# Optimization experiments

Measured on AMD Instinct MI355X. Metric: run time of the kernel, lower is better.

Reference implementation:

```python
import jax, jax.numpy as jnp
import numpy as np


def pairwise_euclidean_distance(x, y):
    # x: [N, D], y: [K, D] -> [N, K] squared Euclidean distances
    cross = -2.0 * (x @ y.T)
    x_term = jnp.sum(x * x, axis=1, keepdims=True)      # [N, 1]
    y_term = jnp.sum(y * y, axis=1, keepdims=True).T    # [1, K]
    return cross + x_term + y_term


def quantize(z, centroids):
    # z: [B, T, D], centroids: [K, D]
    B, T, D = z.shape
    flat = z.reshape(-1, D)                              # [N, D]
    distances = pairwise_euclidean_distance(flat, centroids)
    alignment = jnp.argmin(distances, axis=1)            # [N]
    q = centroids[alignment]                             # gather [N, D]
    # straight-through estimator: grad flows to z, not centroids
    q = flat + jax.lax.stop_gradient(q - flat)
    return q.reshape(B, T, D)


def setup_inputs() -> dict:
    key = jax.random.key(0)
    ks = jax.random.split(key, 5)
    B, T, F, D, K = 16, 2048, 80, 512, 2048
    return {
        "x": jax.random.normal(ks[0], (B, T, F), dtype=jnp.float32),
        "W_enc": jax.random.normal(ks[1], (F, D), dtype=jnp.float32) * (1.0 / np.sqrt(F)),
        "b_enc": jnp.zeros((D,), dtype=jnp.float32),
        "centroids": jax.random.normal(ks[2], (K, D), dtype=jnp.float32),
        "W_dec": jax.random.normal(ks[3], (D, F), dtype=jnp.float32) * (1.0 / np.sqrt(D)),
        "b_dec": jnp.zeros((F,), dtype=jnp.float32),
    }


def reference(x, W_enc, b_enc, centroids, W_dec, b_dec):
    z = x @ W_enc + b_enc            # encoder: [B, T, D]
    zq = quantize(z, centroids)      # VQ: distance + argmin + gather
    out = zq @ W_dec + b_dec         # decoder: [B, T, F]
    return out
```

## Files before the change

### kernel.cpp

```cpp
#include <hip/hip_runtime.h>
#include <hip/hip_bf16.h>

#define N_TOK  32768
#define F_IN   80
#define D_DIM  512
#define K_CENT 2048
#define F_OUT  80
#define TM     16
#define KP     96
#define M2     0.5f
#define QSLOTS 12
#define QREC   104
#define TREC   416

typedef __attribute__((ext_vector_type(8)))  short bf16x8;
typedef __attribute__((ext_vector_type(4)))  float fx4;
typedef __attribute__((ext_vector_type(16))) float fx16;

#define AS3 __attribute__((address_space(3)))
#define AS1 __attribute__((address_space(1)))

__device__ inline unsigned short f2bf(float f) {
    unsigned u = __float_as_uint(f);
    return (unsigned short)((u + 0x7FFFu + ((u >> 16) & 1u)) >> 16);
}
__device__ inline float bf2f(unsigned short h) {
    return __uint_as_float((unsigned)h << 16);
}

__device__ inline void gll16(const unsigned short* g, unsigned short* l) {
    __builtin_amdgcn_global_load_lds((const AS1 unsigned*)g, (AS3 unsigned*)l, 16, 0, 0);
}

__device__ inline unsigned fkey(float f) {
    unsigned b = __float_as_uint(f);
    return b ^ ((b >> 31) ? 0xFFFFFFFFu : 0x80000000u);
}
__device__ inline float keyf(unsigned k) {
    unsigned b = k ^ ((k & 0x80000000u) ? 0x80000000u : 0xFFFFFFFFu);
    return __uint_as_float(b);
}

__device__ inline size_t frag_addr(int row, int k) {
    int stripe = row >> 4;
    int L = ((k >> 3) << 4) + (row & 15);
    return (size_t)stripe * 512 + L * 8 + (k & 7);
}

__device__ inline size_t frag32_addr(int row, int k) {
    int sub = (row >> 5) * 2 + ((k >> 4) & 1);
    int L = (row & 31) + ((k >> 3) & 1) * 32;
    return (size_t)sub * 512 + L * 8 + (k & 7);
}

__global__ void k_prep_all(const float* __restrict__ x, const float* __restrict__ Wenc,
                           const float* __restrict__ cent,
                           unsigned short* __restrict__ cbt, unsigned short* __restrict__ wbt,
                           unsigned short* __restrict__ xbt) {
    const int bid = blockIdx.x, tid = threadIdx.x;
    if (bid < 512) {
        int o = bid * 256 + tid;
        int n = o >> 6, ko = (o & 63) * 8;
        const float* src = cent + (size_t)n * D_DIM + ko;
        float4 v0 = *(const float4*)src;
        float4 v1 = *(const float4*)(src + 4);
        size_t tile = (size_t)((n >> 7) * 16 + (ko >> 5));
        uint4 p;
        p.x = (unsigned)f2bf(v0.x) | ((unsigned)f2bf(v0.y) << 16);
        p.y = (unsigned)f2bf(v0.z) | ((unsigned)f2bf(v0.w) << 16);
        p.z = (unsigned)f2bf(v1.x) | ((unsigned)f2bf(v1.y) << 16);
        p.w = (unsigned)f2bf(v1.z) | ((unsigned)f2bf(v1.w) << 16);
        *(uint4*)&cbt[tile * 4096 + frag_addr(n & 127, ko & 31)] = p;
    } else if (bid < 528) {
        int kt = bid - 512;
        int a0 = tid * 16;
        int s = a0 >> 9;
        int L0 = (tid * 2) & 63;
        int row0 = s * 16 + (L0 & 15);
        int kg = kt * 32 + (L0 >> 4) * 8;
        unsigned short u[16];
#pragma unroll
        for (int rr = 0; rr < 2; ++rr) {
            int row = row0 + rr;
            if (row < F_IN) {
                const float* src = Wenc + (size_t)row * D_DIM + kg;
                float4 v0 = *(const float4*)src;
                float4 v1 = *(const float4*)(src + 4);
                u[rr*8+0]=f2bf(v0.x); u[rr*8+1]=f2bf(v0.y); u[rr*8+2]=f2bf(v0.z); u[rr*8+3]=f2bf(v0.w);
                u[rr*8+4]=f2bf(v1.x); u[rr*8+5]=f2bf(v1.y); u[rr*8+6]=f2bf(v1.z); u[rr*8+7]=f2bf(v1.w);
            } else {
#pragma unroll
                for (int j = 0; j < 8; ++j) u[rr*8+j] = 0;
            }
        }
        unsigned short* dst = wbt + (size_t)kt * 4096 + a0;
#pragma unroll
        for (int j = 0; j < 16; ++j) dst[j] = u[j];
    } else {
        int o = (bid - 528) * 256 + tid;
        int m = o / 12;
        int ko = (o - m * 12) * 8;
        unsigned short u[8];
        if (ko < F_IN) {
            const float* src = x + (size_t)m * F_IN + ko;
            float4 v0 = *(const float4*)src;
            float4 v1 = *(const float4*)(src + 4);
            u[0]=f2bf(v0.x); u[1]=f2bf(v0.y); u[2]=f2bf(v0.z); u[3]=f2bf(v0.w);
            u[4]=f2bf(v1.x); u[5]=f2bf(v1.y); u[6]=f2bf(v1.z); u[7]=f2bf(v1.w);
        } else if (ko == 80) {
            u[0] = 0x3F80; u[1] = 0x3F80;
#pragma unroll
            for (int j = 2; j < 8; ++j) u[j] = 0;
        } else {
#pragma unroll
            for (int j = 0; j < 8; ++j) u[j] = 0;
        }
        int mt = m >> 7, kt = ko >> 5, row = m & 127, kl = ko & 31;
        uint4 p;
        p.x = (unsigned)u[0] | ((unsigned)u[1] << 16);
        p.y = (unsigned)u[2] | ((unsigned)u[3] << 16);
        p.z = (unsigned)u[4] | ((unsigned)u[5] << 16);
        p.w = (unsigned)u[6] | ((unsigned)u[7] << 16);
        *(uint4*)&xbt[(size_t)(mt * 3 + kt) * 4096 + frag32_addr(row, kl)] = p;
    }
}

__global__ __launch_bounds__(512) void k_gemm_g(
    const unsigned short* __restrict__ wbt, const unsigned short* __restrict__ cbt,
    unsigned short* __restrict__ Gbt) {
    __shared__ unsigned short lds[2][2][4096];
    const int tid = threadIdx.x;
    const int nt = blockIdx.x;
    const int lane = tid & 63;
    const int wave = tid >> 6;
    const int wm = wave >> 2, wn = wave & 3;

    const unsigned short* Bbase = cbt + (size_t)nt * 16 * 4096;
    const int woff = (tid & ~63) * 8;

    fx4 acc[4][2] = {};
    gll16(wbt + tid * 8, &lds[0][0][0] + woff);
    gll16(Bbase + tid * 8, &lds[0][1][0] + woff);

    int cur = 0;
    for (int kk = 0; kk < 16; ++kk) {
        __syncthreads();
        if (kk + 1 < 16) {
            gll16(wbt + (kk + 1) * 4096 + tid * 8, &lds[cur ^ 1][0][0] + woff);
            gll16(Bbase + (kk + 1) * 4096 + tid * 8, &lds[cur ^ 1][1][0] + woff);
        }
        const unsigned short* A = &lds[cur][0][0];
        const unsigned short* B = &lds[cur][1][0];
        bf16x8 a[4], b[2];
#pragma unroll
        for (int i = 0; i < 4; ++i) a[i] = *(const bf16x8*)&A[(wm * 4 + i) * 512 + lane * 8];
#pragma unroll
        for (int j = 0; j < 2; ++j) b[j] = *(const bf16x8*)&B[(wn * 2 + j) * 512 + lane * 8];
#pragma unroll
        for (int i = 0; i < 4; ++i)
#pragma unroll
            for (int j = 0; j < 2; ++j)
                acc[i][j] = __builtin_amdgcn_mfma_f32_16x16x32_bf16(a[i], b[j], acc[i][j], 0, 0, 0);
        cur ^= 1;
    }
    const int g = lane >> 4, cl = lane & 15;
#pragma unroll
    for (int j = 0; j < 2; ++j) {
        int colLoc = wn * 32 + j * 16 + cl;
#pragma unroll
        for (int i = 0; i < 4; ++i)
#pragma unroll
            for (int r = 0; r < 4; ++r) {
                int f = wm * 64 + i * 16 + g * 4 + r;
                if (f < KP) {
                    unsigned short v = (f < F_IN) ? f2bf(acc[i][j][r]) : (unsigned short)0;
                    Gbt[(size_t)(nt * 3 + (f >> 5)) * 4096 + frag32_addr(colLoc, f & 31)] = v;
                }
            }
    }
}

__global__ void k_cadjf(const float* __restrict__ cent, const float* __restrict__ benc,
                        float* __restrict__ cnorm, unsigned short* __restrict__ Gbt) {
    int wave = threadIdx.x >> 6, lane = threadIdx.x & 63;
    int k = blockIdx.x * 4 + wave;
    const float* row = cent + (size_t)k * D_DIM;
    float s = 0.f, t = 0.f;
#pragma unroll
    for (int j = 0; j < 8; ++j) {
        float c = row[lane + 64 * j];
        float b = benc[lane + 64 * j];
        s += c * c; t += b * c;
    }
#pragma unroll
    for (int off = 32; off; off >>= 1) { s += __shfl_down(s, off); t += __shfl_down(t, off); }
    if (lane == 0) {
        cnorm[k] = s;
        float v = -0.5f * (s - 2.0f * t);
        unsigned short h = f2bf(v);
        unsigned short l = f2bf(v - bf2f(h));
        int nt = k >> 7, cl = k & 127;
        size_t tb = (size_t)(nt * 3 + 2) * 4096;
        Gbt[tb + frag32_addr(cl, 16)] = h;
        Gbt[tb + frag32_addr(cl, 17)] = l;
    }
}

__global__ __launch_bounds__(256) void k_dec3(
    const float* __restrict__ cent, const float* __restrict__ Wdec,
    const float* __restrict__ bdec, float* __restrict__ dec) {
    __shared__ float cs[4][D_DIM];
    const int tid = threadIdx.x;
    const int k0 = blockIdx.x * 4;
#pragma unroll
    for (int q = 0; q < 2; ++q)
        ((float4*)cs)[q * 256 + tid] = ((const float4*)(cent + (size_t)k0 * D_DIM))[q * 256 + tid];
    __syncthreads();
    const int f = tid & 127, cg = tid >> 7;
    if (f < F_OUT) {
        const int c0 = cg * 2, c1 = cg * 2 + 1;
        float a0 = 0.f, b0 = 0.f, a1 = 0.f, b1 = 0.f;
        const float* wp = Wdec + f;
#pragma unroll 4
        for (int d = 0; d < D_DIM; d += 2) {
            float w0 = wp[(size_t)d * F_OUT];
            float w1 = wp[(size_t)(d + 1) * F_OUT];
            a0 += cs[c0][d] * w0;  b0 += cs[c0][d + 1] * w1;
            a1 += cs[c1][d] * w0;  b1 += cs[c1][d + 1] * w1;
        }
        float bd = bdec[f];
        dec[(size_t)(k0 + c0) * F_OUT + f] = a0 + b0 + bd;
        dec[(size_t)(k0 + c1) * F_OUT + f] = a1 + b1 + bd;
    }
}

__global__ __launch_bounds__(512) void k_dist3(
    const unsigned short* __restrict__ xbt, const unsigned short* __restrict__ Gbt,
    char* __restrict__ lists) {
    __shared__ unsigned short Bs[2][12288];
    __shared__ int cnt[128];
    __shared__ unsigned mxk[128];

    const int tid = threadIdx.x;
    const int bid = blockIdx.x;
    const int mt = bid >> 2, nq = bid & 3;
    const int lane = tid & 63;
    const int wave = tid >> 6;
    const int tg = wave >> 1;
    const int ch = wave & 1;
    const int col = lane & 31;
    const int hi = lane >> 5;

    if (tid < 128) { cnt[tid] = 0; mxk[tid] = 0u; }

    bf16x8 bfr[6];
    const unsigned short* Ab = xbt + (size_t)mt * 12288;
#pragma unroll
    for (int kc = 0; kc < 6; ++kc)
        bfr[kc] = *(const bf16x8*)&Ab[(kc >> 1) * 4096 + (tg * 2 + (kc & 1)) * 512 + lane * 8];

    const int woff = (tid & ~63) * 8;
    const unsigned short* Gq = Gbt + (size_t)nq * 4 * 12288;
#pragma unroll
    for (int q = 0; q < 3; ++q)
        gll16(Gq + q * 4096 + tid * 8, &Bs[0][0] + q * 4096 + woff);

    float rmax = -3.4e38f;
    int cur = 0;
    for (int t4 = 0; t4 < 4; ++t4) {
        __syncthreads();
        if (t4 + 1 < 4) {
#pragma unroll
            for (int q = 0; q < 3; ++q)
                gll16(Gq + (size_t)(t4 + 1) * 12288 + q * 4096 + tid * 8,
                      &Bs[cur ^ 1][0] + q * 4096 + woff);
        }
        const unsigned short* B = &Bs[cur][0];
        fx16 acc[2];
#pragma unroll
        for (int u = 0; u < 2; ++u)
#pragma unroll
            for (int r = 0; r < 16; ++r) acc[u][r] = 0.f;
#pragma unroll
        for (int kc = 0; kc < 6; ++kc) {
#pragma unroll
            for (int u = 0; u < 2; ++u) {
                bf16x8 a = *(const bf16x8*)&B[(kc >> 1) * 4096
                             + ((ch * 2 + u) * 2 + (kc & 1)) * 512 + lane * 8];
                acc[u] = __builtin_amdgcn_mfma_f32_32x32x16_bf16(a, bfr[kc], acc[u], 0, 0, 0);
            }
        }
        float m = acc[0][0];
#pragma unroll
        for (int r = 1; r < 16; ++r) m = fmaxf(m, acc[0][r]);
#pragma unroll
        for (int r = 0; r < 16; ++r) m = fmaxf(m, acc[1][r]);
        m = fmaxf(m, __shfl_xor(m, 32));
        rmax = fmaxf(rmax, m);
        const float th = rmax - M2;
        const int tk = tg * 32 + col;
        char* qrec = lists + (size_t)(mt * 128 + tk) * TREC + nq * QREC;
#pragma unroll
        for (int u = 0; u < 2; ++u)
#pragma unroll
            for (int r = 0; r < 16; ++r) {
                float v = acc[u][r];
                if (v >= th) {
                    int slot = atomicAdd(&cnt[tk], 1);
                    if (slot < QSLOTS) {
                        uint2 e;
                        e.x = __float_as_uint(v);
                        e.y = (unsigned)((nq * 4 + t4) * 128 + (ch * 2 + u) * 32
                                         + (r & 3) + 8 * (r >> 2) + 4 * hi);
                        *(uint2*)(qrec + 8 + slot * 8) = e;
                    }
                }
            }
        cur ^= 1;
    }
    if (lane < 32) atomicMax(&mxk[tg * 32 + lane], fkey(rmax));
    __syncthreads();
    if (tid < 128) {
        uint2 h;
        h.x = (unsigned)cnt[tid];
        h.y = __float_as_uint(keyf(mxk[tid]));
        *(uint2*)(lists + (size_t)(mt * 128 + tid) * TREC + nq * QREC) = h;
    }
}

__global__ __launch_bounds__(256) void k_merge3(
    const char* __restrict__ lists, const float* __restrict__ cnorm,
    const float* __restrict__ cent, const float* __restrict__ x,
    const float* __restrict__ Wenc, const float* __restrict__ benc,
    const float* __restrict__ dec, float* __restrict__ out) {
    const int lane = threadIdx.x & 63;
    const int wid = blockIdx.x * 4 + (threadIdx.x >> 6);
    const int q = lane / 13, s = lane - q * 13;
    for (int it = 0; it < 4; ++it) {
        const int token = wid + it * 8192;
        const char* base = lists + (size_t)token * TREC;
        uint2 w = make_uint2(0u, 0u);
        if (lane < 52) w = *(const uint2*)(base + q * QREC + s * 8);
        const bool ishdr = (lane < 52) && (s == 0);
        float gm = ishdr ? __uint_as_float(w.y) : -3.4e38f;
#pragma unroll
        for (int off = 1; off < 64; off <<= 1) gm = fmaxf(gm, __shfl_xor(gm, off));
        const float th = gm - M2;
        unsigned long long anyovf = __ballot(ishdr && ((int)w.x > QSLOTS));
        int qcnt = __shfl((int)w.x, q * 13);
        int c12 = qcnt < QSLOTS ? qcnt : QSLOTS;
        bool cand = (lane < 52) && (s >= 1) && (s - 1 < c12) && (__uint_as_float(w.x) >= th);
        unsigned long long bal = __ballot(cand);
        int ns = __popcll(bal);
        int ans;
        if (!anyovf && ns == 1) {
            ans = __shfl((int)w.y, __ffsll(bal) - 1);
        } else {
            float z8[8];
#pragma unroll
            for (int j = 0; j < 8; ++j) z8[j] = benc[lane * 8 + j];
            const float* xr = x + (size_t)token * F_IN;
            const float* wp = Wenc + lane * 8;
            for (int f = 0; f < F_IN; ++f) {
                float xf = xr[f];
                fx4 w0 = *(const fx4*)(wp + (size_t)f * D_DIM);
                fx4 w1 = *(const fx4*)(wp + (size_t)f * D_DIM + 4);
                z8[0] += xf * w0.x; z8[1] += xf * w0.y; z8[2] += xf * w0.z; z8[3] += xf * w0.w;
                z8[4] += xf * w1.x; z8[5] += xf * w1.y; z8[6] += xf * w1.z; z8[7] += xf * w1.w;
            }
            float bd = 1e30f; int bn = 0x7FFFFFFF;
            if (!anyovf) {
                unsigned long long m = bal;
                while (m) {
                    int src = __ffsll(m) - 1; m &= m - 1;
                    int ci = __shfl((int)w.y, src);
                    const float* cr = cent + (size_t)ci * D_DIM + lane * 8;
                    fx4 c0 = *(const fx4*)cr, c1 = *(const fx4*)(cr + 4);
                    float dp = z8[0] * c0.x + z8[1] * c0.y + z8[2] * c0.z + z8[3] * c0.w
                             + z8[4] * c1.x + z8[5] * c1.y + z8[6] * c1.z + z8[7] * c1.w;
#pragma unroll
                    for (int off = 1; off < 64; off <<= 1) dp += __shfl_xor(dp, off);
                    float de = cnorm[ci] - 2.0f * dp;
                    if (de < bd || (de == bd && ci < bn)) { bd = de; bn = ci; }
                }
            } else {
                for (int ci = 0; ci < K_CENT; ++ci) {
                    const float* cr = cent + (size_t)ci * D_DIM + lane * 8;
                    fx4 c0 = *(const fx4*)cr, c1 = *(const fx4*)(cr + 4);
                    float dp = z8[0] * c0.x + z8[1] * c0.y + z8[2] * c0.z + z8[3] * c0.w
                             + z8[4] * c1.x + z8[5] * c1.y + z8[6] * c1.z + z8[7] * c1.w;
#pragma unroll
                    for (int off = 1; off < 64; off <<= 1) dp += __shfl_xor(dp, off);
                    float de = cnorm[ci] - 2.0f * dp;
                    if (de < bd || (de == bd && ci < bn)) { bd = de; bn = ci; }
                }
            }
            ans = bn;
        }
        const float* dr = dec + (size_t)ans * F_OUT;
        float* orow = out + (size_t)token * F_OUT;
        orow[lane] = dr[lane];
        if (lane < F_OUT - 64) orow[64 + lane] = dr[64 + lane];
    }
}

__global__ void k_transpose(const float* __restrict__ cent, float* __restrict__ centT) {
    __shared__ float tile[64][65];
    int kb = blockIdx.x * 64, db = blockIdx.y * 64;
    int lx = threadIdx.x & 63, ly = threadIdx.x >> 6;
#pragma unroll
    for (int i = 0; i < 16; ++i) {
        int row = ly + i * 4;
        tile[row][lx] = cent[(size_t)(kb + row) * D_DIM + db + lx];
    }
    __syncthreads();
#pragma unroll
    for (int i = 0; i < 16; ++i) {
        int row = ly + i * 4;
        centT[(size_t)(db + row) * K_CENT + kb + lx] = tile[lx][row];
    }
}

__global__ void k_cnorm(const float* __restrict__ cent, float* __restrict__ cnorm) {
    int wave = threadIdx.x >> 6, lane = threadIdx.x & 63;
    int k = blockIdx.x * 4 + wave;
    const float* row = cent + (size_t)k * D_DIM;
    float s = 0.f;
#pragma unroll
    for (int j = 0; j < 8; ++j) { float v = row[lane + 64 * j]; s += v * v; }
#pragma unroll
    for (int off = 32; off; off >>= 1) s += __shfl_down(s, off);
    if (lane == 0) cnorm[k] = s;
}

__global__ void k_dec(const float* __restrict__ cent, const float* __restrict__ Wdec,
                      const float* __restrict__ bdec, float* __restrict__ dec) {
    __shared__ float cs[D_DIM];
    int k = blockIdx.x;
    for (int d = threadIdx.x; d < D_DIM; d += blockDim.x) cs[d] = cent[(size_t)k * D_DIM + d];
    __syncthreads();
    int f = threadIdx.x;
    if (f < F_OUT) {
        float a0 = 0.f, a1 = 0.f, a2 = 0.f, a3 = 0.f;
#pragma unroll 4
        for (int d = 0; d < D_DIM; d += 4) {
            a0 += cs[d + 0] * Wdec[(d + 0) * F_OUT + f];
            a1 += cs[d + 1] * Wdec[(d + 1) * F_OUT + f];
            a2 += cs[d + 2] * Wdec[(d + 2) * F_OUT + f];
            a3 += cs[d + 3] * Wdec[(d + 3) * F_OUT + f];
        }
        dec[(size_t)k * F_OUT + f] = a0 + a1 + a2 + a3 + bdec[f];
    }
}

__global__ void k_out(const float* __restrict__ dec, const int* __restrict__ idx,
                      float* __restrict__ out) {
    int e0 = blockIdx.x * 2560;
#pragma unroll
    for (int r = 0; r < 10; ++r) {
        int e = e0 + threadIdx.x + r * 256;
        int n = e / F_OUT, f = e - n * F_OUT;
        out[e] = dec[(size_t)idx[n] * F_OUT + f];
    }
}

__global__ __launch_bounds__(256) void k_main(
    const float* __restrict__ x, const float* __restrict__ Wenc,
    const float* __restrict__ benc, const float* __restrict__ centT,
    const float* __restrict__ cnorm, int* __restrict__ idxOut) {
    __shared__ float xs[TM * F_IN];
    __shared__ float zs[TM][D_DIM];
    float* pv = &zs[0][0];
    int*   pi = (int*)(&zs[0][0] + 256 * TM);
    const int tid = threadIdx.x;
    const int tok0 = blockIdx.x * TM;
    for (int e = tid; e < TM * F_IN; e += 256) xs[e] = x[(size_t)tok0 * F_IN + e];
    __syncthreads();
    {
        float acc0[TM], acc1[TM];
#pragma unroll
        for (int t = 0; t < TM; ++t) { acc0[t] = 0.f; acc1[t] = 0.f; }
        const float2 b2 = ((const float2*)benc)[tid];
#pragma unroll 4
        for (int f4 = 0; f4 < F_IN; f4 += 4) {
            float2 w0 = ((const float2*)(Wenc + (size_t)(f4 + 0) * D_DIM))[tid];
            float2 w1 = ((const float2*)(Wenc + (size_t)(f4 + 1) * D_DIM))[tid];
            float2 w2 = ((const float2*)(Wenc + (size_t)(f4 + 2) * D_DIM))[tid];
            float2 w3 = ((const float2*)(Wenc + (size_t)(f4 + 3) * D_DIM))[tid];
#pragma unroll
            for (int t = 0; t < TM; ++t) {
                float4 xv = *(const float4*)&xs[t * F_IN + f4];
                acc0[t] += xv.x * w0.x + xv.y * w1.x + xv.z * w2.x + xv.w * w3.x;
                acc1[t] += xv.x * w0.y + xv.y * w1.y + xv.z * w2.y + xv.w * w3.y;
            }
        }
#pragma unroll
        for (int t = 0; t < TM; ++t)
            *(float2*)&zs[t][2 * tid] = make_float2(acc0[t] + b2.x, acc1[t] + b2.y);
    }
    __syncthreads();
    float minv[TM]; int mini[TM];
#pragma unroll
    for (int t = 0; t < TM; ++t) { minv[t] = 3.4e38f; mini[t] = 0; }
    for (int iter = 0; iter < 2; ++iter) {
        float acc[4][TM];
#pragma unroll
        for (int j = 0; j < 4; ++j)
#pragma unroll
            for (int t = 0; t < TM; ++t) acc[j][t] = 0.f;
        const int cbase = iter * 1024 + tid;
        for (int d4 = 0; d4 < D_DIM; d4 += 4) {
            float cv[4][4];
#pragma unroll
            for (int dd = 0; dd < 4; ++dd) {
                const float* cp = centT + (size_t)(d4 + dd) * K_CENT + cbase;
                cv[dd][0] = cp[0]; cv[dd][1] = cp[256]; cv[dd][2] = cp[512]; cv[dd][3] = cp[768];
            }
#pragma unroll
            for (int t = 0; t < TM; ++t) {
                float4 zv = *(const float4*)&zs[t][d4];
#pragma unroll
                for (int j = 0; j < 4; ++j)
                    acc[j][t] += zv.x * cv[0][j] + zv.y * cv[1][j] + zv.z * cv[2][j] + zv.w * cv[3][j];
            }
        }
#pragma unroll
        for (int j = 0; j < 4; ++j) {
            int c = cbase + j * 256;
            float cn = cnorm[c];
#pragma unroll
            for (int t = 0; t < TM; ++t) {
                float dist = cn - 2.f * acc[j][t];
                if (dist < minv[t]) { minv[t] = dist; mini[t] = c; }
            }
        }
    }
    __syncthreads();
#pragma unroll
    for (int t = 0; t < TM; ++t) { pv[tid * TM + t] = minv[t]; pi[tid * TM + t] = mini[t]; }
    __syncthreads();
    {
        int t = tid & 15, g = tid >> 4;
        float bv = 3.4e38f; int bi = 0x7fffffff;
        for (int j = 0; j < 16; ++j) {
            int r2 = g + 16 * j;
            float vv = pv[r2 * TM + t]; int i2 = pi[r2 * TM + t];
            if (vv < bv || (vv == bv && i2 < bi)) { bv = vv; bi = i2; }
        }
        pv[g * TM + t] = bv; pi[g * TM + t] = bi;
    }
    __syncthreads();
    if (tid < TM) {
        int t = tid;
        float bv = 3.4e38f; int bi = 0x7fffffff;
        for (int g = 0; g < 16; ++g) {
            float vv = pv[g * TM + t]; int i2 = pi[g * TM + t];
            if (vv < bv || (vv == bv && i2 < bi)) { bv = vv; bi = i2; }
        }
        idxOut[tok0 + t] = bi;
    }
}

extern "C" void kernel_launch(void* const* d_in, const int* in_sizes, int n_in,
                              void* d_out, int out_size, void* d_ws, size_t ws_size,
                              hipStream_t stream) {
    const float* x    = (const float*)d_in[0];
    const float* Wenc = (const float*)d_in[1];
    const float* benc = (const float*)d_in[2];
    const float* cent = (const float*)d_in[3];
    const float* Wdec = (const float*)d_in[4];
    const float* bdec = (const float*)d_in[5];
    float* out = (float*)d_out;

    const size_t L_B  = (size_t)N_TOK * TREC;
    const size_t XB_B = (size_t)N_TOK * KP * 2;
    const size_t CB_B = (size_t)K_CENT * D_DIM * 2;
    const size_t WB_B = (size_t)128 * D_DIM * 2;
    const size_t GB_B = (size_t)K_CENT * KP * 2;
    const size_t N_B  = (size_t)K_CENT * 4;
    const size_t D_B  = (size_t)K_CENT * F_OUT * 4;
    const size_t NEED = L_B + XB_B + CB_B + WB_B + GB_B + N_B + D_B;

    if (ws_size >= NEED) {
        char* w = (char*)d_ws;
        char*           lists = w;                            w += L_B;
        unsigned short* xbt   = (unsigned short*)w;           w += XB_B;
        unsigned short* cbt   = (unsigned short*)w;           w += CB_B;
        unsigned short* wbt   = (unsigned short*)w;           w += WB_B;
        unsigned short* Gbt   = (unsigned short*)w;           w += GB_B;
        float*          cnorm = (float*)w;                    w += N_B;
        float*          dec   = (float*)w;

        k_prep_all<<<2064, 256, 0, stream>>>(x, Wenc, cent, cbt, wbt, xbt);
        k_gemm_g<<<16, 512, 0, stream>>>(wbt, cbt, Gbt);
        k_cadjf<<<K_CENT / 4, 256, 0, stream>>>(cent, benc, cnorm, Gbt);
        k_dec3<<<K_CENT / 4, 256, 0, stream>>>(cent, Wdec, bdec, dec);
        k_dist3<<<1024, 512, 0, stream>>>(xbt, Gbt, lists);
        k_merge3<<<2048, 256, 0, stream>>>(lists, cnorm, cent, x, Wenc, benc, dec, out);
    } else {
        float* centT = (float*)d_ws;
        float* cnorm = centT + (size_t)D_DIM * K_CENT;
        float* dec   = cnorm + K_CENT;
        int*   idx   = (int*)(dec + (size_t)K_CENT * F_OUT);
        k_transpose<<<dim3(K_CENT / 64, D_DIM / 64), 256, 0, stream>>>(cent, centT);
        k_cnorm<<<K_CENT / 4, 256, 0, stream>>>(cent, cnorm);
        k_dec<<<K_CENT, 128, 0, stream>>>(cent, Wdec, bdec, dec);
        k_main<<<N_TOK / TM, 256, 0, stream>>>(x, Wenc, benc, centT, cnorm, idx);
        k_out<<<N_TOK * F_OUT / 2560, 256, 0, stream>>>(dec, idx, out);
    }
}
```

Before: 105.6 us.

## Fuse centroid prep, G projection, norms and decoder table into one kernel

Replaces four preprocessing launches (bf16 conversion of centroids and Wenc, MFMA GEMM for G, centroid norms/bias terms, decoder table) with a single kernel. Blocks with index below 1536 convert x, and the remaining 512 blocks each load four centroids into shared memory and compute the norm, the G = centroids·Wencᵀ rows in fp32 scalar dot products, and the decoder rows. This removes three launch overheads and the cbt/wbt intermediate buffers. In exchange, the G projection moves from MFMA to scalar FMAs and adds Wenc re-reads per block.

Result: slower. 177.4 us (+67.9%).

```diff
diff --git a/kernel.cpp b/kernel.cpp
--- a/kernel.cpp
+++ b/kernel.cpp
@@ -41,63 +41,21 @@
     return __uint_as_float(b);
 }
 
-__device__ inline size_t frag_addr(int row, int k) {
-    int stripe = row >> 4;
-    int L = ((k >> 3) << 4) + (row & 15);
-    return (size_t)stripe * 512 + L * 8 + (k & 7);
-}
-
 __device__ inline size_t frag32_addr(int row, int k) {
     int sub = (row >> 5) * 2 + ((k >> 4) & 1);
     int L = (row & 31) + ((k >> 3) & 1) * 32;
     return (size_t)sub * 512 + L * 8 + (k & 7);
 }
 
-__global__ void k_prep_all(const float* __restrict__ x, const float* __restrict__ Wenc,
-                           const float* __restrict__ cent,
-                           unsigned short* __restrict__ cbt, unsigned short* __restrict__ wbt,
-                           unsigned short* __restrict__ xbt) {
+__global__ __launch_bounds__(256) void k_prep2(
+    const float* __restrict__ x, const float* __restrict__ Wenc,
+    const float* __restrict__ benc, const float* __restrict__ cent,
+    const float* __restrict__ Wdec, const float* __restrict__ bdec,
+    unsigned short* __restrict__ xbt, unsigned short* __restrict__ Gbt,
+    float* __restrict__ cnorm, float* __restrict__ dec) {
     const int bid = blockIdx.x, tid = threadIdx.x;
-    if (bid < 512) {
+    if (bid < 1536) {
         int o = bid * 256 + tid;
-        int n = o >> 6, ko = (o & 63) * 8;
-        const float* src = cent + (size_t)n * D_DIM + ko;
-        float4 v0 = *(const float4*)src;
-        float4 v1 = *(const float4*)(src + 4);
-        size_t tile = (size_t)((n >> 7) * 16 + (ko >> 5));
-        uint4 p;
-        p.x = (unsigned)f2bf(v0.x) | ((unsigned)f2bf(v0.y) << 16);
-        p.y = (unsigned)f2bf(v0.z) | ((unsigned)f2bf(v0.w) << 16);
-        p.z = (unsigned)f2bf(v1.x) | ((unsigned)f2bf(v1.y) << 16);
-        p.w = (unsigned)f2bf(v1.z) | ((unsigned)f2bf(v1.w) << 16);
-        *(uint4*)&cbt[tile * 4096 + frag_addr(n & 127, ko & 31)] = p;
-    } else if (bid < 528) {
-        int kt = bid - 512;
-        int a0 = tid * 16;
-        int s = a0 >> 9;
-        int L0 = (tid * 2) & 63;
-        int row0 = s * 16 + (L0 & 15);
-        int kg = kt * 32 + (L0 >> 4) * 8;
-        unsigned short u[16];
-#pragma unroll
-        for (int rr = 0; rr < 2; ++rr) {
-            int row = row0 + rr;
-            if (row < F_IN) {
-                const float* src = Wenc + (size_t)row * D_DIM + kg;
-                float4 v0 = *(const float4*)src;
-                float4 v1 = *(const float4*)(src + 4);
-                u[rr*8+0]=f2bf(v0.x); u[rr*8+1]=f2bf(v0.y); u[rr*8+2]=f2bf(v0.z); u[rr*8+3]=f2bf(v0.w);
-                u[rr*8+4]=f2bf(v1.x); u[rr*8+5]=f2bf(v1.y); u[rr*8+6]=f2bf(v1.z); u[rr*8+7]=f2bf(v1.w);
-            } else {
-#pragma unroll
-                for (int j = 0; j < 8; ++j) u[rr*8+j] = 0;
-            }
-        }
-        unsigned short* dst = wbt + (size_t)kt * 4096 + a0;
-#pragma unroll
-        for (int j = 0; j < 16; ++j) dst[j] = u[j];
-    } else {
-        int o = (bid - 528) * 256 + tid;
         int m = o / 12;
         int ko = (o - m * 12) * 8;
         unsigned short u[8];
@@ -122,115 +80,74 @@
         p.z = (unsigned)u[4] | ((unsigned)u[5] << 16);
         p.w = (unsigned)u[6] | ((unsigned)u[7] << 16);
         *(uint4*)&xbt[(size_t)(mt * 3 + kt) * 4096 + frag32_addr(row, kl)] = p;
-    }
-}
-
-__global__ __launch_bounds__(512) void k_gemm_g(
-    const unsigned short* __restrict__ wbt, const unsigned short* __restrict__ cbt,
-    unsigned short* __restrict__ Gbt) {
-    __shared__ unsigned short lds[2][2][4096];
-    const int tid = threadIdx.x;
-    const int nt = blockIdx.x;
-    const int lane = tid & 63;
-    const int wave = tid >> 6;
-    const int wm = wave >> 2, wn = wave & 3;
-
-    const unsigned short* Bbase = cbt + (size_t)nt * 16 * 4096;
-    const int woff = (tid & ~63) * 8;
-
-    fx4 acc[4][2] = {};
-    gll16(wbt + tid * 8, &lds[0][0][0] + woff);
-    gll16(Bbase + tid * 8, &lds[0][1][0] + woff);
-
-    int cur = 0;
-    for (int kk = 0; kk < 16; ++kk) {
-        __syncthreads();
-        if (kk + 1 < 16) {
-            gll16(wbt + (kk + 1) * 4096 + tid * 8, &lds[cur ^ 1][0][0] + woff);
-            gll16(Bbase + (kk + 1) * 4096 + tid * 8, &lds[cur ^ 1][1][0] + woff);
-        }
-        const unsigned short* A = &lds[cur][0][0];
-        const unsigned short* B = &lds[cur][1][0];
-        bf16x8 a[4], b[2];
-#pragma unroll
-        for (int i = 0; i < 4; ++i) a[i] = *(const bf16x8*)&A[(wm * 4 + i) * 512 + lane * 8];
-#pragma unroll
-        for (int j = 0; j < 2; ++j) b[j] = *(const bf16x8*)&B[(wn * 2 + j) * 512 + lane * 8];
-#pragma unroll
-        for (int i = 0; i < 4; ++i)
-#pragma unroll
-            for (int j = 0; j < 2; ++j)
-                acc[i][j] = __builtin_amdgcn_mfma_f32_16x16x32_bf16(a[i], b[j], acc[i][j], 0, 0, 0);
-        cur ^= 1;
-    }
-    const int g = lane >> 4, cl = lane & 15;
-#pragma unroll
-    for (int j = 0; j < 2; ++j) {
-        int colLoc = wn * 32 + j * 16 + cl;
-#pragma unroll
-        for (int i = 0; i < 4; ++i)
-#pragma unroll
-            for (int r = 0; r < 4; ++r) {
-                int f = wm * 64 + i * 16 + g * 4 + r;
-                if (f < KP) {
-                    unsigned short v = (f < F_IN) ? f2bf(acc[i][j][r]) : (unsigned short)0;
-                    Gbt[(size_t)(nt * 3 + (f >> 5)) * 4096 + frag32_addr(colLoc, f & 31)] = v;
-                }
-            }
-    }
-}
-
-__global__ void k_cadjf(const float* __restrict__ cent, const float* __restrict__ benc,
-                        float* __restrict__ cnorm, unsigned short* __restrict__ Gbt) {
-    int wave = threadIdx.x >> 6, lane = threadIdx.x & 63;
-    int k = blockIdx.x * 4 + wave;
-    const float* row = cent + (size_t)k * D_DIM;
-    float s = 0.f, t = 0.f;
-#pragma unroll
-    for (int j = 0; j < 8; ++j) {
-        float c = row[lane + 64 * j];
-        float b = benc[lane + 64 * j];
-        s += c * c; t += b * c;
-    }
-#pragma unroll
-    for (int off = 32; off; off >>= 1) { s += __shfl_down(s, off); t += __shfl_down(t, off); }
-    if (lane == 0) {
-        cnorm[k] = s;
-        float v = -0.5f * (s - 2.0f * t);
-        unsigned short h = f2bf(v);
-        unsigned short l = f2bf(v - bf2f(h));
-        int nt = k >> 7, cl = k & 127;
-        size_t tb = (size_t)(nt * 3 + 2) * 4096;
-        Gbt[tb + frag32_addr(cl, 16)] = h;
-        Gbt[tb + frag32_addr(cl, 17)] = l;
-    }
-}
-
-__global__ __launch_bounds__(256) void k_dec3(
-    const float* __restrict__ cent, const float* __restrict__ Wdec,
-    const float* __restrict__ bdec, float* __restrict__ dec) {
+        return;
+    }
     __shared__ float cs[4][D_DIM];
-    const int tid = threadIdx.x;
-    const int k0 = blockIdx.x * 4;
+    const int k0 = (bid - 1536) * 4;
 #pragma unroll
     for (int q = 0; q < 2; ++q)
         ((float4*)cs)[q * 256 + tid] = ((const float4*)(cent + (size_t)k0 * D_DIM))[q * 256 + tid];
     __syncthreads();
-    const int f = tid & 127, cg = tid >> 7;
-    if (f < F_OUT) {
-        const int c0 = cg * 2, c1 = cg * 2 + 1;
-        float a0 = 0.f, b0 = 0.f, a1 = 0.f, b1 = 0.f;
-        const float* wp = Wdec + f;
+
+    const int c = tid >> 6, lane = tid & 63;
+    const int k = k0 + c;
+    const int nt = k >> 7, cl = k & 127;
+
+    {
+        float s = 0.f, t = 0.f;
+#pragma unroll
+        for (int j = 0; j < 8; ++j) {
+            float cv = cs[c][lane + 64 * j];
+            float b  = benc[lane + 64 * j];
+            s += cv * cv; t += b * cv;
+        }
+#pragma unroll
+        for (int off = 32; off; off >>= 1) { s += __shfl_down(s, off); t += __shfl_down(t, off); }
+        if (lane == 0) {
+            cnorm[k] = s;
+            float v = -0.5f * (s - 2.0f * t);
+            unsigned short h = f2bf(v);
+            unsigned short l = f2bf(v - bf2f(h));
+            size_t tb = (size_t)(nt * 3 + 2) * 4096;
+            Gbt[tb + frag32_addr(cl, 16)] = h;
+            Gbt[tb + frag32_addr(cl, 17)] = l;
+        }
+    }
+
+#pragma unroll
+    for (int fr = 0; fr < 2; ++fr) {
+        int f = lane + fr * 64;
+        if (f < F_IN) {
+            const float* wr = Wenc + (size_t)f * D_DIM;
+            float a0 = 0.f, a1 = 0.f, a2 = 0.f, a3 = 0.f;
+            for (int d = 0; d < D_DIM; d += 4) {
+                float4 wv = *(const float4*)(wr + d);
+                fx4 cv = *(const fx4*)&cs[c][d];
+                a0 += wv.x * cv.x; a1 += wv.y * cv.y;
+                a2 += wv.z * cv.z; a3 += wv.w * cv.w;
+            }
+            Gbt[(size_t)(nt * 3 + (f >> 5)) * 4096 + frag32_addr(cl, f & 31)]
+                = f2bf(a0 + a1 + a2 + a3);
+        } else if (f >= 82 && f < KP) {
+            Gbt[(size_t)(nt * 3 + 2) * 4096 + frag32_addr(cl, f & 31)] = 0;
+        }
+    }
+
+#pragma unroll
+    for (int fr = 0; fr < 2; ++fr) {
+        int fo = lane + fr * 64;
+        if (fo < F_OUT) {
+            float a0 = 0.f, a1 = 0.f, a2 = 0.f, a3 = 0.f;
+            const float* wp = Wdec + fo;
 #pragma unroll 4
-        for (int d = 0; d < D_DIM; d += 2) {
-            float w0 = wp[(size_t)d * F_OUT];
-            float w1 = wp[(size_t)(d + 1) * F_OUT];
-            a0 += cs[c0][d] * w0;  b0 += cs[c0][d + 1] * w1;
-            a1 += cs[c1][d] * w0;  b1 += cs[c1][d + 1] * w1;
-        }
-        float bd = bdec[f];
-        dec[(size_t)(k0 + c0) * F_OUT + f] = a0 + b0 + bd;
-        dec[(size_t)(k0 + c1) * F_OUT + f] = a1 + b1 + bd;
+            for (int d = 0; d < D_DIM; d += 4) {
+                a0 += cs[c][d + 0] * wp[(size_t)(d + 0) * F_OUT];
+                a1 += cs[c][d + 1] * wp[(size_t)(d + 1) * F_OUT];
+                a2 += cs[c][d + 2] * wp[(size_t)(d + 2) * F_OUT];
+                a3 += cs[c][d + 3] * wp[(size_t)(d + 3) * F_OUT];
+            }
+            dec[(size_t)k * F_OUT + fo] = a0 + a1 + a2 + a3 + bdec[fo];
+        }
     }
 }
 
@@ -574,27 +491,21 @@
 
     const size_t L_B  = (size_t)N_TOK * TREC;
     const size_t XB_B = (size_t)N_TOK * KP * 2;
-    const size_t CB_B = (size_t)K_CENT * D_DIM * 2;
-    const size_t WB_B = (size_t)128 * D_DIM * 2;
     const size_t GB_B = (size_t)K_CENT * KP * 2;
     const size_t N_B  = (size_t)K_CENT * 4;
     const size_t D_B  = (size_t)K_CENT * F_OUT * 4;
-    const size_t NEED = L_B + XB_B + CB_B + WB_B + GB_B + N_B + D_B;
+    const size_t NEED = L_B + XB_B + GB_B + N_B + D_B;
 
     if (ws_size >= NEED) {
         char* w = (char*)d_ws;
         char*           lists = w;                            w += L_B;
         unsigned short* xbt   = (unsigned short*)w;           w += XB_B;
-        unsigned short* cbt   = (unsigned short*)w;           w += CB_B;
-        unsigned short* wbt   = (unsigned short*)w;           w += WB_B;
         unsigned short* Gbt   = (unsigned short*)w;           w += GB_B;
         float*          cnorm = (float*)w;                    w += N_B;
         float*          dec   = (float*)w;
 
-        k_prep_all<<<2064, 256, 0, stream>>>(x, Wenc, cent, cbt, wbt, xbt);
-        k_gemm_g<<<16, 512, 0, stream>>>(wbt, cbt, Gbt);
-        k_cadjf<<<K_CENT / 4, 256, 0, stream>>>(cent, benc, cnorm, Gbt);
-        k_dec3<<<K_CENT / 4, 256, 0, stream>>>(cent, Wdec, bdec, dec);
+        k_prep2<<<2048, 256, 0, stream>>>(x, Wenc, benc, cent, Wdec, bdec,
+                                          xbt, Gbt, cnorm, dec);
         k_dist3<<<1024, 512, 0, stream>>>(xbt, Gbt, lists);
         k_merge3<<<2048, 256, 0, stream>>>(lists, cnorm, cent, x, Wenc, benc, dec, out);
     } else {
```
